# Kernel optimization log

Hardware: AMD Instinct MI355X
Metric: run time of the kernel (lower is better)

## Reference

```python
import jax, jax.numpy as jnp
import numpy as np

B, C, L, H = 4, 128, 4096, 4
GROUPS, EPS = 32, 1e-5


def group_norm(x, gamma, beta):
    # x: [B, C, L]; normalize per (batch, group) over (C//G, L)
    b, c, l = x.shape
    xg = x.reshape(b, GROUPS, c // GROUPS, l)
    mu = jnp.mean(xg, axis=(2, 3), keepdims=True)
    var = jnp.var(xg, axis=(2, 3), keepdims=True)
    xn = ((xg - mu) * jax.lax.rsqrt(var + EPS)).reshape(b, c, l)
    return xn * gamma[None, :, None] + beta[None, :, None]


def setup_inputs() -> dict:
    key = jax.random.key(0)
    k1, k2, k3 = jax.random.split(key, 3)
    return {
        "x": jax.random.normal(k1, (B, C, L), dtype=jnp.float32),
        "w_qkv": jax.random.normal(k2, (3 * C, C), dtype=jnp.float32) * 0.02,
        "w_proj": jax.random.normal(k3, (C, C), dtype=jnp.float32) * 0.02,
        "b_proj": jnp.zeros((C,), dtype=jnp.float32),
        "gn_gamma": jnp.ones((C,), dtype=jnp.float32),
        "gn_beta": jnp.zeros((C,), dtype=jnp.float32),
    }


def reference(x, w_qkv, w_proj, b_proj, gn_gamma, gn_beta):
    b, c, l = x.shape
    hd = c // H
    h = group_norm(x, gn_gamma, gn_beta)
    # 1x1 conv == channel matmul: [B, 3C, L]
    qkv = jnp.einsum('oc,bcl->bol', w_qkv, h)
    # torch reshape(B*H, 3C/H, L).chunk(3, dim=1): per-head contiguous slices
    qkv = qkv.reshape(b, H, 3 * hd, l)
    q, k, v = qkv[:, :, :hd], qkv[:, :, hd:2 * hd], qkv[:, :, 2 * hd:]
    scale = 1.0 / np.sqrt(np.sqrt(hd)).astype(np.float32)
    attn = jnp.einsum('bhct,bhcs->bhts', q * scale, k * scale)
    attn = jax.nn.softmax(attn, axis=-1)
    o = jnp.einsum('bhts,bhcs->bhct', attn, v).reshape(b, c, l)
    o = jnp.einsum('oc,bcl->bol', w_proj, o) + b_proj[None, :, None]
    return o + x
```

## Files before the change

### kernel.cpp

```cpp
#include <hip/hip_runtime.h>
#include <hip/hip_bf16.h>
#include <cstdint>
#include <cstddef>


#define B_ 4
#define C_ 128
#define L_ 4096
#define H_ 4
#define HD_ 32
#define NG_ 32
#define CPG_ 4
#define EPS_ 1e-5f
#define QKSCALE_ 0.5050097650430367f

typedef __attribute__((ext_vector_type(8))) short bf16x8;
typedef __attribute__((ext_vector_type(8))) unsigned short u16x8;
typedef __attribute__((ext_vector_type(4))) float f32x4;
typedef __attribute__((ext_vector_type(2))) _Float16 f16x2;
typedef __attribute__((ext_vector_type(4))) _Float16 f16x4;

#if __has_builtin(__builtin_amdgcn_exp2f)
#define EXP2F(x) __builtin_amdgcn_exp2f(x)
#else
#define EXP2F(x) exp2f(x)
#endif

#define MFMA_PV(a, b, c) __builtin_amdgcn_mfma_f32_16x16x16f16((a), (b), (c), 0, 0, 0)

__device__ __forceinline__ float bu2f(unsigned short u) {
  return __builtin_bit_cast(float, (unsigned int)(((unsigned int)u) << 16));
}
__device__ __forceinline__ unsigned short f2bu(float f) {
  unsigned int u = __builtin_bit_cast(unsigned int, f);
  unsigned int r = (u + 0x7fffu + ((u >> 16) & 1u)) >> 16;
  return (unsigned short)r;
}
__device__ __forceinline__ float4 u42f4(ushort4 u) {
  return make_float4(bu2f(u.x), bu2f(u.y), bu2f(u.z), bu2f(u.w));
}
__device__ __forceinline__ unsigned int pkbf(float a, float b) {
  return (unsigned int)f2bu(a) | ((unsigned int)f2bu(b) << 16);
}
__device__ __forceinline__ f16x2 pkhf2(float a, float b) {
#if __has_builtin(__builtin_amdgcn_cvt_pkrtz)
  return __builtin_bit_cast(f16x2, __builtin_amdgcn_cvt_pkrtz(a, b));
#else
  f16x2 r;
  r[0] = (_Float16)a;
  r[1] = (_Float16)b;
  return r;
#endif
}
__device__ __forceinline__ unsigned int pkhf(float a, float b) {
  return __builtin_bit_cast(unsigned int, pkhf2(a, b));
}

__device__ __forceinline__ void gload16(const void* g, void* l) {
  __builtin_amdgcn_global_load_lds(
      (const __attribute__((address_space(1))) unsigned int*)g,
      (__attribute__((address_space(3))) unsigned int*)l, 16, 0, 0);
}

__device__ __forceinline__ bool detect_fast(const ushort* x) {
  __shared__ int flag_s;
  int t = threadIdx.x;
  if (t < 64) {
    int e = (x[t] >> 7) & 0xFF;
    unsigned long long m = __ballot((e < 64) || (e > 192));
    if (t == 0) flag_s = (__popcll(m) > 4) ? 1 : 0;
  }
  __syncthreads();
  return flag_s != 0;
}

__device__ __forceinline__ float4 ldx4(const void* x, size_t idx, bool f32) {
  if (f32) return *((const float4*)x + (idx >> 2));
  ushort4 u = *((const ushort4*)x + (idx >> 2));
  return u42f4(u);
}

__global__ __launch_bounds__(256) void gn_stats(const void* __restrict__ x,
                                                const void* __restrict__ wq,
                                                const void* __restrict__ wp,
                                                const void* __restrict__ bp,
                                                const void* __restrict__ gm,
                                                const void* __restrict__ bt,
                                                ushort* __restrict__ wq_b,
                                                ushort* __restrict__ wp_b,
                                                float* __restrict__ bp_f,
                                                float2* __restrict__ gn_ab) {
  bool f32 = detect_fast((const ushort*)x);
  int blk = blockIdx.x;
  int t = threadIdx.x;

  if (blk >= 128) {
    int i0 = ((blk - 128) * 256 + t) * 8;
#pragma unroll
    for (int k = 0; k < 8; ++k) {
      int i = i0 + k;
      if (i >= 65664) break;
      if (i < 49152) {
        wq_b[i] = f32 ? f2bu(((const float*)wq)[i]) : ((const ushort*)wq)[i];
      } else if (i < 65536) {
        int off = i - 49152;
        wp_b[off] = f32 ? f2bu(((const float*)wp)[off]) : ((const ushort*)wp)[off];
      } else {
        int off = i - 65536;
        bp_f[off] = f32 ? ((const float*)bp)[off] : bu2f(((const ushort*)bp)[off]);
      }
    }
    return;
  }

  int b = blk >> 5, g = blk & 31;
  size_t base = ((size_t)b * C_ + (size_t)g * CPG_) * L_;

  float s = 0.f, ss = 0.f;
#pragma unroll
  for (int i = 0; i < 16; ++i) {
    size_t e = base + i * 1024 + t * 4;
    float4 f = ldx4(x, e, f32);
    s += f.x + f.y + f.z + f.w;
    ss += f.x * f.x + f.y * f.y + f.z * f.z + f.w * f.w;
  }
#pragma unroll
  for (int m = 32; m >= 1; m >>= 1) {
    s += __shfl_xor(s, m, 64);
    ss += __shfl_xor(ss, m, 64);
  }
  __shared__ float red[4][2];
  int wv = t >> 6;
  if ((t & 63) == 0) { red[wv][0] = s; red[wv][1] = ss; }
  __syncthreads();
  float ts = red[0][0] + red[1][0] + red[2][0] + red[3][0];
  float tss = red[0][1] + red[1][1] + red[2][1] + red[3][1];
  float mu = ts * (1.0f / 16384.0f);
  float var = tss * (1.0f / 16384.0f) - mu * mu;
  float rs = rsqrtf(var + EPS_);

  if (t < CPG_) {
    int gi = g * CPG_ + t;
    float ga = f32 ? ((const float*)gm)[gi] : bu2f(((const ushort*)gm)[gi]);
    float be = f32 ? ((const float*)bt)[gi] : bu2f(((const ushort*)bt)[gi]);
    gn_ab[b * C_ + gi] = make_float2(ga * rs, be - mu * ga * rs);
  }
}

__global__ __launch_bounds__(256) void qkv_kernel(const ushort* __restrict__ wq_b,
                                                  const void* __restrict__ x,
                                                  const float2* __restrict__ gn_ab,
                                                  ushort* __restrict__ Qt,
                                                  ushort* __restrict__ Kt,
                                                  ushort* __restrict__ Vb) {
  bool f32 = detect_fast((const ushort*)x);
  __shared__ alignas(16) ushort Hs[64][136];
  __shared__ alignas(16) float Ls[64][69];

  int lx = blockIdx.x, oz = blockIdx.y, b = blockIdx.z;
  int t = threadIdx.x;
  int w = t >> 6, lane = t & 63, l16 = lane & 15, q = lane >> 4, q8 = q * 8;

  {
    int u = t & 63, lh = (t >> 6) * 16;
    int c0 = 2 * u;
    float2 ab0 = gn_ab[b * C_ + c0];
    float2 ab1 = gn_ab[b * C_ + c0 + 1];
    size_t xo = ((size_t)b * C_ + c0) * L_ + (size_t)lx * 64 + lh;
#pragma unroll
    for (int j = 0; j < 4; ++j) {
      float4 f0 = ldx4(x, xo + j * 4, f32);
      float4 f1 = ldx4(x, xo + L_ + j * 4, f32);
      float n0[4] = {f0.x * ab0.x + ab0.y, f0.y * ab0.x + ab0.y,
                     f0.z * ab0.x + ab0.y, f0.w * ab0.x + ab0.y};
      float n1[4] = {f1.x * ab1.x + ab1.y, f1.y * ab1.x + ab1.y,
                     f1.z * ab1.x + ab1.y, f1.w * ab1.x + ab1.y};
#pragma unroll
      for (int k = 0; k < 4; ++k)
        *(unsigned int*)&Hs[lh + j * 4 + k][c0] = pkbf(n0[k], n1[k]);
    }
  }
  __syncthreads();

  for (int j = 0; j < 2; ++j) {
    int oy = oz * 2 + j;
    const ushort* wg = wq_b + (size_t)(oy * 64 + w * 16 + l16) * C_;

    f32x4 acc[4] = {{0.f, 0.f, 0.f, 0.f}, {0.f, 0.f, 0.f, 0.f},
                    {0.f, 0.f, 0.f, 0.f}, {0.f, 0.f, 0.f, 0.f}};
#pragma unroll
    for (int kc = 0; kc < 4; ++kc) {
      bf16x8 aw = *(const bf16x8*)(wg + kc * 32 + q8);
#pragma unroll
      for (int nb = 0; nb < 4; ++nb) {
        bf16x8 bh = *(const bf16x8*)&Hs[nb * 16 + l16][kc * 32 + q8];
        acc[nb] = __builtin_amdgcn_mfma_f32_16x16x32_bf16(aw, bh, acc[nb], 0, 0, 0);
      }
    }
    __syncthreads();
#pragma unroll
    for (int nb = 0; nb < 4; ++nb)
#pragma unroll
      for (int r = 0; r < 4; ++r)
        Ls[nb * 16 + l16][w * 16 + 4 * q + r] = acc[nb][r];
    __syncthreads();

#pragma unroll
    for (int hhalf = 0; hhalf < 2; ++hhalf) {
      int hh = oy * 2 + hhalf;
      int type = hh % 3, head = hh / 3;
      size_t bh = (size_t)b * H_ + head;
      if (type == 2) {
        int c_loc = t >> 3, l8 = (t & 7) * 8;
        float v[8];
#pragma unroll
        for (int jj = 0; jj < 8; ++jj) v[jj] = Ls[l8 + jj][hhalf * 32 + c_loc];
        uint4 u;
        u.x = pkhf(v[0], v[1]);
        u.y = pkhf(v[2], v[3]);
        u.z = pkhf(v[4], v[5]);
        u.w = pkhf(v[6], v[7]);
        *(uint4*)(Vb + (bh * 32 + c_loc) * L_ + (size_t)lx * 64 + l8) = u;
      } else {
        ushort* dst = type ? Kt : Qt;
        int l = t >> 2, seg = (t & 3) * 8;
        const float* src = &Ls[l][hhalf * 32 + seg];
        uint4 u;
        u.x = pkbf(src[0] * QKSCALE_, src[1] * QKSCALE_);
        u.y = pkbf(src[2] * QKSCALE_, src[3] * QKSCALE_);
        u.z = pkbf(src[4] * QKSCALE_, src[5] * QKSCALE_);
        u.w = pkbf(src[6] * QKSCALE_, src[7] * QKSCALE_);
        *(uint4*)(dst + ((bh * L_) + lx * 64 + l) * 32 + seg) = u;
      }
    }
  }
}

__global__ __launch_bounds__(512) void attn_kernel(const ushort* __restrict__ Qt,
                                                   const ushort* __restrict__ Kt,
                                                   const ushort* __restrict__ Vb,
                                                   ushort* __restrict__ ot) {
  __shared__ alignas(16) ushort Ks[2][4096];
  __shared__ alignas(16) ushort Vs[2][32][128];

  int t = threadIdx.x;
  int w = t >> 6, lane = t & 63, l16 = lane & 15, q = lane >> 4;
  int q8 = q * 8, q4 = q * 4;
  int trow = w * 16 + l16;
  int tq0 = blockIdx.x * 128;
  int bh = blockIdx.y;
  int b = bh >> 2, head = bh & 3;
  const ushort* Qg = Qt + ((size_t)bh * L_ + tq0) * 32;
  const ushort* Kg = Kt + (size_t)bh * L_ * 32;
  const ushort* Vg = Vb + (size_t)bh * 32 * L_;

  {
  }
  int j = t & 255;
  int krow = ((j & 15) | ((j >> 6) << 4)) + ((t >> 8) << 6);
  int kq8s = ((j >> 4) & 3) * 8;
  const ushort* ksrc = Kg + (size_t)krow * 32 + kq8s;
  int vr = t >> 4, vp = t & 15;
  int vcsem = (vp & 8) | ((vp & 7) ^ (vr & 7));
  const ushort* vsrc = Vg + (size_t)vr * L_ + vcsem * 8;

  ushort* kA = (ushort*)Ks + (size_t)t * 8;
  ushort* kB = kA + 4096;
  ushort* vA = (ushort*)Vs + (size_t)t * 8;
  ushort* vB = vA + 4096;

  bf16x8 qfrag = *(const bf16x8*)(Qg + (size_t)trow * 32 + q8);
  f16x4 ones;
#pragma unroll
  for (int i = 0; i < 4; ++i) ones[i] = (_Float16)1.0f;

  gload16(ksrc, kA);
  gload16(vsrc, vA);
  ksrc += 4096;
  vsrc += 128;
  __syncthreads();

  f32x4 aA = {0.f, 0.f, 0.f, 0.f};
  f32x4 aB = {0.f, 0.f, 0.f, 0.f};
  f32x4 aL = {0.f, 0.f, 0.f, 0.f};

  int flip = 0;
  for (int it = 0; it < 32; ++it) {
    if (it < 31) {
      gload16(ksrc, flip ? kA : kB);
      gload16(vsrc, flip ? vA : vB);
      ksrc += 4096;
      vsrc += 128;
    }
    const ushort* kc = (const ushort*)Ks + (flip ? 4096 : 0);
    const ushort* vc = (const ushort*)Vs + (flip ? 4096 : 0);

#pragma unroll
    for (int hh2 = 0; hh2 < 2; ++hh2) {
      const ushort* kf = kc + hh2 * 2048 + lane * 8;
      bf16x8 ak0 = *(const bf16x8*)(kf);
      bf16x8 ak1 = *(const bf16x8*)(kf + 512);
      bf16x8 ak2 = *(const bf16x8*)(kf + 1024);
      bf16x8 ak3 = *(const bf16x8*)(kf + 1536);
      f32x4 z = {0.f, 0.f, 0.f, 0.f};
      f32x4 sf[4];
      __builtin_amdgcn_s_setprio(1);
      sf[0] = __builtin_amdgcn_mfma_f32_16x16x32_bf16(ak0, qfrag, z, 0, 0, 0);
      sf[1] = __builtin_amdgcn_mfma_f32_16x16x32_bf16(ak1, qfrag, z, 0, 0, 0);
      sf[2] = __builtin_amdgcn_mfma_f32_16x16x32_bf16(ak2, qfrag, z, 0, 0, 0);
      sf[3] = __builtin_amdgcn_mfma_f32_16x16x32_bf16(ak3, qfrag, z, 0, 0, 0);
      __builtin_amdgcn_s_setprio(0);

#pragma unroll
      for (int n = 0; n < 4; ++n) {
        int o = hh2 * 64 + n * 16 + q4;
        int c = o >> 3;
        int pch = (c & 8) | ((c & 7) ^ (l16 & 7));
        const ushort* vrow = vc + pch * 8 + (q4 & 7);
        f16x4 va0 = *(const f16x4*)(vrow + (size_t)l16 * 128);
        f16x4 va1 = *(const f16x4*)(vrow + (size_t)(16 + l16) * 128);
        float p0 = EXP2F(sf[n][0]);
        float p1 = EXP2F(sf[n][1]);
        float p2 = EXP2F(sf[n][2]);
        float p3 = EXP2F(sf[n][3]);
        f16x2 e01 = pkhf2(p0, p1);
        f16x2 e23 = pkhf2(p2, p3);
        f16x4 pb = __builtin_shufflevector(e01, e23, 0, 1, 2, 3);
        aA = MFMA_PV(va0, pb, aA);
        aB = MFMA_PV(va1, pb, aB);
        aL = MFMA_PV(ones, pb, aL);
      }
    }
    __syncthreads();
    flip ^= 1;
  }

  float inv = 1.0f / aL[0];

  ushort* Ep = (ushort*)Ks;
#pragma unroll
  for (int r = 0; r < 2; ++r) {
    *(unsigned int*)&Ep[trow * 40 + q4 + 2 * r] =
        pkbf(aA[2 * r] * inv, aA[2 * r + 1] * inv);
    *(unsigned int*)&Ep[trow * 40 + 16 + q4 + 2 * r] =
        pkbf(aB[2 * r] * inv, aB[2 * r + 1] * inv);
  }
  __syncthreads();
  {
    int row = t >> 2, seg = (t & 3) * 8;
    *(uint4*)(ot + ((size_t)b * L_ + tq0 + row) * C_ + head * 32 + seg) =
        *(const uint4*)&Ep[row * 40 + seg];
  }
}

__global__ __launch_bounds__(256) void proj_kernel(const ushort* __restrict__ wp_b,
                                                   const float* __restrict__ bias,
                                                   const void* __restrict__ x,
                                                   const ushort* __restrict__ ot,
                                                   void* __restrict__ out) {
  bool f32 = detect_fast((const ushort*)x);
  __shared__ alignas(16) float Ls[64][37];

  int lx = blockIdx.x, oy = blockIdx.y, b = blockIdx.z;
  int t = threadIdx.x;
  int w = t >> 6, lane = t & 63, l16 = lane & 15, q = lane >> 4, q8 = q * 8;

  const ushort* wg = wp_b + (size_t)(oy * 64 + w * 16 + l16) * C_;
  const ushort* og = ot + ((size_t)b * L_ + (size_t)lx * 32) * C_;

  f32x4 acc[2] = {{0.f, 0.f, 0.f, 0.f}, {0.f, 0.f, 0.f, 0.f}};
#pragma unroll
  for (int kc = 0; kc < 4; ++kc) {
    bf16x8 aw = *(const bf16x8*)(wg + kc * 32 + q8);
#pragma unroll
    for (int nb = 0; nb < 2; ++nb) {
      bf16x8 bo = *(const bf16x8*)(og + (size_t)(nb * 16 + l16) * C_ + kc * 32 + q8);
      acc[nb] = __builtin_amdgcn_mfma_f32_16x16x32_bf16(aw, bo, acc[nb], 0, 0, 0);
    }
  }
#pragma unroll
  for (int nb = 0; nb < 2; ++nb)
#pragma unroll
    for (int r = 0; r < 4; ++r)
      Ls[w * 16 + 4 * q + r][nb * 16 + l16] = acc[nb][r];
  __syncthreads();

  {
    int o_loc = t >> 2, ls0 = (t & 3) * 8;
    float bv = bias[oy * 64 + o_loc];
    size_t off = ((size_t)b * C_ + oy * 64 + o_loc) * L_ + (size_t)lx * 32 + ls0;
#pragma unroll
    for (int jj = 0; jj < 2; ++jj) {
      float4 xf = ldx4(x, off + jj * 4, f32);
      const float* sp = &Ls[o_loc][ls0 + jj * 4];
      float4 r = make_float4(sp[0] + bv + xf.x, sp[1] + bv + xf.y,
                             sp[2] + bv + xf.z, sp[3] + bv + xf.w);
      if (f32) {
        *(float4*)((float*)out + off + jj * 4) = r;
      } else {
        *(ushort4*)((ushort*)out + off + jj * 4) =
            make_ushort4(f2bu(r.x), f2bu(r.y), f2bu(r.z), f2bu(r.w));
      }
    }
  }
}

extern "C" void kernel_launch(void* const* d_in, const int* in_sizes, int n_in,
                              void* d_out, int out_size, void* d_ws, size_t ws_size,
                              hipStream_t stream) {
  const void* x      = d_in[0];
  const void* w_qkv  = d_in[1];
  const void* w_proj = d_in[2];
  const void* b_proj = d_in[3];
  const void* gamma  = d_in[4];
  const void* beta   = d_in[5];

  char* wsb = (char*)d_ws;
  ushort* wq_b  = (ushort*)(wsb + 0);
  ushort* wp_b  = (ushort*)(wsb + 98304);
  float*  bp_f  = (float*)(wsb + 131072);
  float2* gn_ab = (float2*)(wsb + 131584);
  ushort* Qt    = (ushort*)(wsb + 8388608);
  ushort* Kt    = (ushort*)(wsb + 12582912);
  ushort* Vb    = (ushort*)(wsb + 16777216);
  ushort* ot    = (ushort*)(wsb + 20971520);

  gn_stats<<<dim3(161), dim3(256), 0, stream>>>(x, w_qkv, w_proj, b_proj, gamma, beta,
                                                wq_b, wp_b, bp_f, gn_ab);
  qkv_kernel<<<dim3(L_ / 64, 3, B_), dim3(256), 0, stream>>>(wq_b, x, gn_ab, Qt, Kt, Vb);
  attn_kernel<<<dim3(L_ / 128, B_ * H_), dim3(512), 0, stream>>>(Qt, Kt, Vb, ot);
  proj_kernel<<<dim3(L_ / 32, C_ / 64, B_), dim3(256), 0, stream>>>(wp_b, bp_f, x, ot, d_out);
}
```

Baseline: 144.3 us.

## Rewrite attention inner loop with 32x32 MFMA tiles and split-key reduction

The attention kernel now uses 32x32x16 MFMA for both QK^T and PV, with each wave covering 32 queries over half of every key tile. The two halves are combined through shared memory at the end. Row sums are accumulated with fdot2 instead of a third ones-MFMA, and the P fragments are rearranged with permlane32_swap so they can feed the PV MFMA directly. This is meant to cut MFMA instruction count and the redundant row-sum MFMA, at the cost of a larger LDS epilogue, a cross-wave reduction, and a new K swizzle layout.

```diff
diff --git a/kernel.cpp b/kernel.cpp
--- a/kernel.cpp
+++ b/kernel.cpp
@@ -17,16 +17,18 @@
 typedef __attribute__((ext_vector_type(8))) short bf16x8;
 typedef __attribute__((ext_vector_type(8))) unsigned short u16x8;
 typedef __attribute__((ext_vector_type(4))) float f32x4;
+typedef __attribute__((ext_vector_type(16))) float f32x16;
 typedef __attribute__((ext_vector_type(2))) _Float16 f16x2;
 typedef __attribute__((ext_vector_type(4))) _Float16 f16x4;
+typedef __attribute__((ext_vector_type(8))) _Float16 f16x8;
+typedef __attribute__((ext_vector_type(2))) unsigned int u32x2;
+typedef __attribute__((ext_vector_type(4))) unsigned int u32x4;
 
 #if __has_builtin(__builtin_amdgcn_exp2f)
 #define EXP2F(x) __builtin_amdgcn_exp2f(x)
 #else
 #define EXP2F(x) exp2f(x)
 #endif
-
-#define MFMA_PV(a, b, c) __builtin_amdgcn_mfma_f32_16x16x16f16((a), (b), (c), 0, 0, 0)
 
 __device__ __forceinline__ float bu2f(unsigned short u) {
   return __builtin_bit_cast(float, (unsigned int)(((unsigned int)u) << 16));
@@ -236,17 +238,15 @@
   }
 }
 
-__global__ __launch_bounds__(512) void attn_kernel(const ushort* __restrict__ Qt,
-                                                   const ushort* __restrict__ Kt,
-                                                   const ushort* __restrict__ Vb,
-                                                   ushort* __restrict__ ot) {
-  __shared__ alignas(16) ushort Ks[2][4096];
-  __shared__ alignas(16) ushort Vs[2][32][128];
+__global__ __launch_bounds__(512, 6) void attn_kernel(const ushort* __restrict__ Qt,
+                                                      const ushort* __restrict__ Kt,
+                                                      const ushort* __restrict__ Vb,
+                                                      ushort* __restrict__ ot) {
+  __shared__ alignas(16) char smem[35840];
 
   int t = threadIdx.x;
-  int w = t >> 6, lane = t & 63, l16 = lane & 15, q = lane >> 4;
-  int q8 = q * 8, q4 = q * 4;
-  int trow = w * 16 + l16;
+  int w = t >> 6, lane = t & 63, l31 = lane & 31, hi = lane >> 5;
+  int qt = w & 3, sh = w >> 2;
   int tq0 = blockIdx.x * 128;
   int bh = blockIdx.y;
   int b = bh >> 2, head = bh & 3;
@@ -254,102 +254,126 @@
   const ushort* Kg = Kt + (size_t)bh * L_ * 32;
   const ushort* Vg = Vb + (size_t)bh * 32 * L_;
 
-  {
-  }
-  int j = t & 255;
-  int krow = ((j & 15) | ((j >> 6) << 4)) + ((t >> 8) << 6);
-  int kq8s = ((j >> 4) & 3) * 8;
-  const ushort* ksrc = Kg + (size_t)krow * 32 + kq8s;
+  int rd = t >> 2, pd = t & 3;
+  int kcsem = (pd - rd) & 3;
+  const ushort* ksrc = Kg + (size_t)rd * 32 + kcsem * 8;
   int vr = t >> 4, vp = t & 15;
   int vcsem = (vp & 8) | ((vp & 7) ^ (vr & 7));
   const ushort* vsrc = Vg + (size_t)vr * L_ + vcsem * 8;
 
-  ushort* kA = (ushort*)Ks + (size_t)t * 8;
-  ushort* kB = kA + 4096;
-  ushort* vA = (ushort*)Vs + (size_t)t * 8;
-  ushort* vB = vA + 4096;
-
-  bf16x8 qfrag = *(const bf16x8*)(Qg + (size_t)trow * 32 + q8);
-  f16x4 ones;
-#pragma unroll
-  for (int i = 0; i < 4; ++i) ones[i] = (_Float16)1.0f;
-
-  gload16(ksrc, kA);
-  gload16(vsrc, vA);
+  char* kb0 = smem;
+  char* kb1 = smem + 8192;
+  char* vb0 = smem + 16384;
+  char* vb1 = smem + 24576;
+
+  const ushort* qbase = Qg + (size_t)(qt * 32 + l31) * 32;
+  bf16x8 qB0 = *(const bf16x8*)(qbase + 8 * hi);
+  bf16x8 qB1 = *(const bf16x8*)(qbase + 16 + 8 * hi);
+
+  const f16x2 one2 = {(_Float16)1.0f, (_Float16)1.0f};
+
+  gload16(ksrc, kb0 + (size_t)t * 16);
+  gload16(vsrc, vb0 + (size_t)t * 16);
   ksrc += 4096;
   vsrc += 128;
   __syncthreads();
 
-  f32x4 aA = {0.f, 0.f, 0.f, 0.f};
-  f32x4 aB = {0.f, 0.f, 0.f, 0.f};
-  f32x4 aL = {0.f, 0.f, 0.f, 0.f};
+  f32x16 aO = {0.f};
+  float lsum = 0.f;
 
   int flip = 0;
   for (int it = 0; it < 32; ++it) {
     if (it < 31) {
-      gload16(ksrc, flip ? kA : kB);
-      gload16(vsrc, flip ? vA : vB);
+      gload16(ksrc, (flip ? kb0 : kb1) + (size_t)t * 16);
+      gload16(vsrc, (flip ? vb0 : vb1) + (size_t)t * 16);
       ksrc += 4096;
       vsrc += 128;
     }
-    const ushort* kc = (const ushort*)Ks + (flip ? 4096 : 0);
-    const ushort* vc = (const ushort*)Vs + (flip ? 4096 : 0);
-
-#pragma unroll
-    for (int hh2 = 0; hh2 < 2; ++hh2) {
-      const ushort* kf = kc + hh2 * 2048 + lane * 8;
-      bf16x8 ak0 = *(const bf16x8*)(kf);
-      bf16x8 ak1 = *(const bf16x8*)(kf + 512);
-      bf16x8 ak2 = *(const bf16x8*)(kf + 1024);
-      bf16x8 ak3 = *(const bf16x8*)(kf + 1536);
-      f32x4 z = {0.f, 0.f, 0.f, 0.f};
-      f32x4 sf[4];
+    const ushort* kc = (const ushort*)(flip ? kb1 : kb0);
+    const ushort* vc = (const ushort*)(flip ? vb1 : vb0);
+
+#pragma unroll
+    for (int st = 0; st < 2; ++st) {
+      int s0 = 64 * sh + 32 * st;
+      const ushort* krow = kc + (size_t)(s0 + l31) * 32;
+      bf16x8 aK0 = *(const bf16x8*)(krow + ((hi + l31) & 3) * 8);
+      bf16x8 aK1 = *(const bf16x8*)(krow + ((2 + hi + l31) & 3) * 8);
+      f32x16 zz = {0.f};
+      f32x16 sf;
       __builtin_amdgcn_s_setprio(1);
-      sf[0] = __builtin_amdgcn_mfma_f32_16x16x32_bf16(ak0, qfrag, z, 0, 0, 0);
-      sf[1] = __builtin_amdgcn_mfma_f32_16x16x32_bf16(ak1, qfrag, z, 0, 0, 0);
-      sf[2] = __builtin_amdgcn_mfma_f32_16x16x32_bf16(ak2, qfrag, z, 0, 0, 0);
-      sf[3] = __builtin_amdgcn_mfma_f32_16x16x32_bf16(ak3, qfrag, z, 0, 0, 0);
+      sf = __builtin_amdgcn_mfma_f32_32x32x16_bf16(aK0, qB0, zz, 0, 0, 0);
+      sf = __builtin_amdgcn_mfma_f32_32x32x16_bf16(aK1, qB1, sf, 0, 0, 0);
       __builtin_amdgcn_s_setprio(0);
 
 #pragma unroll
-      for (int n = 0; n < 4; ++n) {
-        int o = hh2 * 64 + n * 16 + q4;
-        int c = o >> 3;
-        int pch = (c & 8) | ((c & 7) ^ (l16 & 7));
-        const ushort* vrow = vc + pch * 8 + (q4 & 7);
-        f16x4 va0 = *(const f16x4*)(vrow + (size_t)l16 * 128);
-        f16x4 va1 = *(const f16x4*)(vrow + (size_t)(16 + l16) * 128);
-        float p0 = EXP2F(sf[n][0]);
-        float p1 = EXP2F(sf[n][1]);
-        float p2 = EXP2F(sf[n][2]);
-        float p3 = EXP2F(sf[n][3]);
-        f16x2 e01 = pkhf2(p0, p1);
-        f16x2 e23 = pkhf2(p2, p3);
-        f16x4 pb = __builtin_shufflevector(e01, e23, 0, 1, 2, 3);
-        aA = MFMA_PV(va0, pb, aA);
-        aB = MFMA_PV(va1, pb, aB);
-        aL = MFMA_PV(ones, pb, aL);
+      for (int sb = 0; sb < 2; ++sb) {
+        int sblk = 4 * sh + 2 * st + sb;
+        int kci = 2 * sblk + hi;
+        int vpos = (kci & 8) | ((kci & 7) ^ (l31 & 7));
+        f16x8 vf = *(const f16x8*)(vc + (size_t)l31 * 128 + vpos * 8);
+
+        float p0 = EXP2F(sf[8 * sb + 0]);
+        float p1 = EXP2F(sf[8 * sb + 1]);
+        float p2 = EXP2F(sf[8 * sb + 2]);
+        float p3 = EXP2F(sf[8 * sb + 3]);
+        float p4 = EXP2F(sf[8 * sb + 4]);
+        float p5 = EXP2F(sf[8 * sb + 5]);
+        float p6 = EXP2F(sf[8 * sb + 6]);
+        float p7 = EXP2F(sf[8 * sb + 7]);
+        f16x2 cA0 = pkhf2(p0, p1), cA1 = pkhf2(p2, p3);
+        f16x2 cB0 = pkhf2(p4, p5), cB1 = pkhf2(p6, p7);
+        lsum = __builtin_amdgcn_fdot2(cA0, one2, lsum, false);
+        lsum = __builtin_amdgcn_fdot2(cA1, one2, lsum, false);
+        lsum = __builtin_amdgcn_fdot2(cB0, one2, lsum, false);
+        lsum = __builtin_amdgcn_fdot2(cB1, one2, lsum, false);
+
+        u32x2 r0 = __builtin_amdgcn_permlane32_swap(
+            __builtin_bit_cast(unsigned int, cA0),
+            __builtin_bit_cast(unsigned int, cB0), false, false);
+        u32x2 r1 = __builtin_amdgcn_permlane32_swap(
+            __builtin_bit_cast(unsigned int, cA1),
+            __builtin_bit_cast(unsigned int, cB1), false, false);
+        u32x4 pw = {r0.x, r1.x, r0.y, r1.y};
+        f16x8 pf = __builtin_bit_cast(f16x8, pw);
+
+        __builtin_amdgcn_s_setprio(1);
+        aO = __builtin_amdgcn_mfma_f32_32x32x16_f16(vf, pf, aO, 0, 0, 0);
+        __builtin_amdgcn_s_setprio(0);
       }
     }
     __syncthreads();
     flip ^= 1;
   }
 
-  float inv = 1.0f / aL[0];
-
-  ushort* Ep = (ushort*)Ks;
-#pragma unroll
-  for (int r = 0; r < 2; ++r) {
-    *(unsigned int*)&Ep[trow * 40 + q4 + 2 * r] =
-        pkbf(aA[2 * r] * inv, aA[2 * r + 1] * inv);
-    *(unsigned int*)&Ep[trow * 40 + 16 + q4 + 2 * r] =
-        pkbf(aB[2 * r] * inv, aB[2 * r + 1] * inv);
-  }
-  __syncthreads();
+  float* Osh = (float*)smem;
+  float* Lp = (float*)(smem + 33792);
   {
-    int row = t >> 2, seg = (t & 3) * 8;
-    *(uint4*)(ot + ((size_t)b * L_ + tq0 + row) * C_ + head * 32 + seg) =
-        *(const uint4*)&Ep[row * 40 + seg];
+    float* ob = Osh + (size_t)(sh * 4 + qt) * (32 * 33) + (size_t)l31 * 33;
+#pragma unroll
+    for (int reg = 0; reg < 16; ++reg) {
+      int R = (reg & 3) + 8 * (reg >> 2) + 4 * hi;
+      ob[R] = aO[reg];
+    }
+    Lp[(sh * 2 + hi) * 128 + qt * 32 + l31] = lsum;
+  }
+  __syncthreads();
+
+  {
+    int qloc = t >> 2, c0 = (t & 3) * 8;
+    int qt2 = qloc >> 5, q31 = qloc & 31;
+    float lt = Lp[qloc] + Lp[128 + qloc] + Lp[256 + qloc] + Lp[384 + qloc];
+    float inv = 1.0f / lt;
+    const float* o0 = Osh + (size_t)qt2 * (32 * 33) + (size_t)q31 * 33 + c0;
+    const float* o1 = o0 + 4 * (32 * 33);
+    float o[8];
+#pragma unroll
+    for (int jj = 0; jj < 8; ++jj) o[jj] = (o0[jj] + o1[jj]) * inv;
+    uint4 u;
+    u.x = pkbf(o[0], o[1]);
+    u.y = pkbf(o[2], o[3]);
+    u.z = pkbf(o[4], o[5]);
+    u.w = pkbf(o[6], o[7]);
+    *(uint4*)(ot + ((size_t)b * L_ + tq0 + qloc) * C_ + head * 32 + c0) = u;
   }
 }
 
```

After: 138.5 us. 4.0% less time.
